# Optimization experiments

Hardware: AMD Instinct MI355X
Metric: run time of the kernel (lower is better)

## Reference

```python
import jax, jax.numpy as jnp
import numpy as np

B, S, D = 4, 4096, 768

def setup_inputs() -> dict:
    key = jax.random.key(0)
    kx, kq, kk, kv = jax.random.split(key, 4)
    x = jax.random.normal(kx, (B, S, D), dtype=jnp.float32)
    Wq = jax.random.normal(kq, (D, D), dtype=jnp.float32) * (D ** -0.5)
    Wk = jax.random.normal(kk, (D, D), dtype=jnp.float32) * (D ** -0.5)
    Wv = jax.random.normal(kv, (D, D), dtype=jnp.float32) * (D ** -0.5)
    return {"x": x, "Wq": Wq, "Wk": Wk, "Wv": Wv}

def reference(x, Wq, Wk, Wv):
    # q,k,v: [B,S,D]  (Linear with no bias)
    q = x @ Wq
    k = x @ Wk
    v = x @ Wv
    # full N x N causal score matrix, as in the original module
    scores = jnp.einsum('bqd,bkd->bqk', q, k)  # [B,S,S]
    seq = scores.shape[1]
    causal_mask = jnp.triu(jnp.ones((seq, seq), dtype=bool), k=1)  # True above diagonal
    scores = jnp.where(causal_mask[None, :, :], -jnp.inf, scores)
    scale = jnp.asarray(k.shape[-1], scores.dtype) ** 0.5
    weights = jax.nn.softmax(scores / scale, axis=-1)  # [B,S,S]
    # dropout p=0.0 -> identity (deterministic reference)
    context = jnp.einsum('bqk,bkd->bqd', weights, v)  # [B,S,D]
    return context
```

## Files before the change

kernel.cpp:

```cpp
#include <hip/hip_runtime.h>
#include <hip/hip_bf16.h>

typedef __attribute__((ext_vector_type(8))) _Float16 half8_t;
typedef __attribute__((ext_vector_type(4))) _Float16 half4_t;
typedef __attribute__((ext_vector_type(4))) float float4_t;

#define D_DIM 768
#define S_DIM 4096
#define B_DIM 4
#define M_DIM (B_DIM * S_DIM)
#define SD ((size_t)S_DIM * D_DIM)

#define GLOAD_LDS16(g, s)                                      \
  __builtin_amdgcn_global_load_lds(                            \
      (const __attribute__((address_space(1))) void*)(g),      \
      (__attribute__((address_space(3))) void*)(s), 16, 0, 0)

__device__ __forceinline__ float4_t mfma16(half8_t a, half8_t b, float4_t c) {
  return __builtin_amdgcn_mfma_f32_16x16x32_f16(a, b, c, 0, 0, 0);
}

__global__ __launch_bounds__(256) void cvt_x_kernel(const float* __restrict__ in,
                                                    _Float16* __restrict__ out, int n) {
  int i = (blockIdx.x * 256 + threadIdx.x) * 4;
  if (i < n) {
    float4 v = *(const float4*)(in + i);
    half4_t o;
    o.x = (_Float16)v.x; o.y = (_Float16)v.y; o.z = (_Float16)v.z; o.w = (_Float16)v.w;
    *(half4_t*)(out + i) = o;
  }
}

__global__ __launch_bounds__(256) void transpose_w_kernel(const float* __restrict__ W0,
                                                          const float* __restrict__ W1,
                                                          const float* __restrict__ W2,
                                                          _Float16* __restrict__ WT) {
  const float* W = (blockIdx.z == 0) ? W0 : (blockIdx.z == 1) ? W1 : W2;
  _Float16* o = WT + (size_t)blockIdx.z * D_DIM * D_DIM;
  __shared__ _Float16 tile[64][68];
  int k0 = blockIdx.x * 64, n0 = blockIdx.y * 64;
#pragma unroll
  for (int i = 0; i < 16; ++i) {
    int idx = threadIdx.x + i * 256;
    int r = idx >> 6, c = idx & 63;
    tile[r][c] = (_Float16)W[(size_t)(k0 + r) * D_DIM + n0 + c];
  }
  __syncthreads();
#pragma unroll
  for (int i = 0; i < 16; ++i) {
    int idx = threadIdx.x + i * 256;
    int r = idx >> 6, c = idx & 63;
    o[(size_t)(n0 + r) * D_DIM + k0 + c] = tile[c][r];
  }
}

template <bool SWAP>
__device__ __forceinline__ void core256p(const _Float16* __restrict__ Ag,
                                         const _Float16* __restrict__ Bg,
                                         int lda, int ldb, int nt,
                                         char* lds, float4_t (&acc)[8][4]) {
  const int tid = threadIdx.x;
  const int w = tid >> 6, l = tid & 63;
  const int wm = w >> 2, wn = w & 3;
  const int l15 = l & 15, l4 = l >> 4;

  int sRow[2], sU[2], sDst[2];
#pragma unroll
  for (int i = 0; i < 2; ++i) {
    int L = i * 512 + tid;
    int row = L >> 3, u = L & 7;
    sRow[i] = row;
    sU[i] = (u ^ (row & 7)) * 8;
    sDst[i] = (i * 512 + (tid & ~63)) * 16;
  }

  const int a7 = l15 & 7;
  const int kt0 = ((0 * 4 + l4) ^ a7) * 16;
  const int kt1 = ((1 * 4 + l4) ^ a7) * 16;
  const int aBase = (wm * 128 + l15) * 128;
  const int bBase = 32768 + (wn * 64 + l15) * 128;

#define STGP(t)                                                                 \
  do {                                                                          \
    char* base = lds + ((t) & 1) * 65536;                                       \
    const _Float16* As = Ag + (size_t)(t) * 64;                                 \
    const _Float16* Bs = Bg + (size_t)(t) * 64;                                 \
    _Pragma("unroll") for (int i = 0; i < 2; ++i)                               \
        GLOAD_LDS16(As + (size_t)sRow[i] * lda + sU[i], base + sDst[i]);        \
    _Pragma("unroll") for (int i = 0; i < 2; ++i)                               \
        GLOAD_LDS16(As + (size_t)(sRow[i] + 128) * lda + sU[i],                 \
                    base + 16384 + sDst[i]);                                    \
    _Pragma("unroll") for (int i = 0; i < 2; ++i)                               \
        GLOAD_LDS16(Bs + (size_t)sRow[i] * ldb + sU[i], base + 32768 + sDst[i]);\
    _Pragma("unroll") for (int i = 0; i < 2; ++i)                               \
        GLOAD_LDS16(Bs + (size_t)(sRow[i] + 128) * ldb + sU[i],                 \
                    base + 49152 + sDst[i]);                                    \
  } while (0)

  STGP(0);

#pragma unroll 1
  for (int t = 0; t < nt; ++t) {
    asm volatile("s_waitcnt vmcnt(0)" ::: "memory");
    __builtin_amdgcn_s_barrier();
    __builtin_amdgcn_sched_barrier(0);
    if (t + 1 < nt) STGP(t + 1);
    __builtin_amdgcn_sched_barrier(0);

    const char* Lb = lds + (t & 1) * 65536;
    const char* pA0 = Lb + aBase + kt0;
    const char* pA1 = Lb + aBase + kt1;
    const char* pB0 = Lb + bBase + kt0;
    const char* pB1 = Lb + bBase + kt1;

    half8_t bf[4][2];
#pragma unroll
    for (int ni = 0; ni < 4; ++ni) {
      bf[ni][0] = *(const half8_t*)(pB0 + ni * 2048);
      bf[ni][1] = *(const half8_t*)(pB1 + ni * 2048);
    }

#pragma unroll
    for (int q = 0; q < 4; ++q) {
      if (q) {
        __builtin_amdgcn_s_barrier();
        __builtin_amdgcn_sched_barrier(0);
      }
      half8_t af[2][2];
#pragma unroll
      for (int di = 0; di < 2; ++di) {
        af[di][0] = *(const half8_t*)(pA0 + (q * 2 + di) * 2048);
        af[di][1] = *(const half8_t*)(pA1 + (q * 2 + di) * 2048);
      }
      __builtin_amdgcn_s_setprio(1);
#pragma unroll
      for (int di = 0; di < 2; ++di)
#pragma unroll
        for (int ni = 0; ni < 4; ++ni)
#pragma unroll
          for (int ks = 0; ks < 2; ++ks) {
            if (SWAP)
              acc[q * 2 + di][ni] = mfma16(bf[ni][ks], af[di][ks], acc[q * 2 + di][ni]);
            else
              acc[q * 2 + di][ni] = mfma16(af[di][ks], bf[ni][ks], acc[q * 2 + di][ni]);
          }
      __builtin_amdgcn_s_setprio(0);
    }
    __builtin_amdgcn_s_barrier();
  }
#undef STGP
}

template <bool SWAP>
__device__ __forceinline__ void core128(const _Float16* __restrict__ Ag,
                                        const _Float16* __restrict__ Bg,
                                        int lda, int ldb, int nt,
                                        char* lds, float4_t (&acc)[4][4]) {
  const int tid = threadIdx.x;
  const int w = tid >> 6, l = tid & 63;
  const int wr = w >> 1, wc = w & 1;
  const int l15 = l & 15, l4 = l >> 4;

  int sA[4], sB[4], sDst[4];
#pragma unroll
  for (int i = 0; i < 4; ++i) {
    int L = i * 256 + tid;
    int row = L >> 3, u = L & 7;
    int usw = u ^ (row & 7);
    sA[i] = row * lda + usw * 8;
    sB[i] = row * ldb + usw * 8;
    sDst[i] = (i * 256 + (tid & ~63)) * 16;
  }

  int aOff[2][4], bOff[2][4];
#pragma unroll
  for (int ks = 0; ks < 2; ++ks) {
#pragma unroll
    for (int i = 0; i < 4; ++i) {
      int ar = wr * 64 + i * 16 + l15;
      aOff[ks][i] = ar * 128 + (((ks * 4 + l4) ^ (ar & 7)) * 16);
      int br = wc * 64 + i * 16 + l15;
      bOff[ks][i] = 16384 + br * 128 + (((ks * 4 + l4) ^ (br & 7)) * 16);
    }
  }

#pragma unroll 1
  for (int kt = 0; kt < nt; ++kt) {
#pragma unroll
    for (int i = 0; i < 4; ++i)
      GLOAD_LDS16(Ag + (size_t)kt * 64 + sA[i], lds + sDst[i]);
#pragma unroll
    for (int i = 0; i < 4; ++i)
      GLOAD_LDS16(Bg + (size_t)kt * 64 + sB[i], lds + 16384 + sDst[i]);
    __syncthreads();
#pragma unroll
    for (int ks = 0; ks < 2; ++ks) {
      half8_t af[4], bf[4];
#pragma unroll
      for (int ni = 0; ni < 4; ++ni) bf[ni] = *(const half8_t*)(lds + bOff[ks][ni]);
#pragma unroll
      for (int mi = 0; mi < 4; ++mi) af[mi] = *(const half8_t*)(lds + aOff[ks][mi]);
      __builtin_amdgcn_s_setprio(1);
#pragma unroll
      for (int mi = 0; mi < 4; ++mi)
#pragma unroll
        for (int ni = 0; ni < 4; ++ni) {
          if (SWAP)
            acc[mi][ni] = mfma16(bf[ni], af[mi], acc[mi][ni]);
          else
            acc[mi][ni] = mfma16(af[mi], bf[ni], acc[mi][ni]);
        }
      __builtin_amdgcn_s_setprio(0);
    }
    __syncthreads();
  }
}

__global__ __launch_bounds__(512) void proj8_kernel(const _Float16* __restrict__ xh,
                                                    const _Float16* __restrict__ WT,
                                                    _Float16* __restrict__ qkv,
                                                    _Float16* __restrict__ vt) {
  __shared__ __align__(16) char lds[131072];
  const int bid = blockIdx.x;
  const int wid = (bid & 7) * 72 + (bid >> 3);
  const int rg2 = wid / 18;
  const int rem = wid % 18;
  const int z = rem / 6;
  const int cb = (rem % 6) >> 1;
  const int rbg = rg2 * 2 + (rem & 1);

  const _Float16* Ag = xh + (size_t)rbg * 256 * D_DIM;
  const _Float16* Bg = WT + (size_t)z * D_DIM * D_DIM + (size_t)cb * 256 * D_DIM;
  float4_t acc[8][4];
#pragma unroll
  for (int a = 0; a < 8; ++a)
#pragma unroll
    for (int b = 0; b < 4; ++b) acc[a][b] = (float4_t){0.f, 0.f, 0.f, 0.f};

  const int tid = threadIdx.x;
  const int w = tid >> 6, l = tid & 63;
  const int wr = w >> 2, wc = w & 3;
  const int l15 = l & 15, l4 = l >> 4;

  if (z < 2) {
    core256p<false>(Ag, Bg, D_DIM, D_DIM, 12, lds, acc);
    _Float16* C = qkv + (size_t)z * M_DIM * D_DIM;
#pragma unroll
    for (int mi = 0; mi < 8; ++mi)
#pragma unroll
      for (int ni = 0; ni < 4; ++ni) {
        int col = cb * 256 + wc * 64 + ni * 16 + l15;
#pragma unroll
        for (int j = 0; j < 4; ++j) {
          int row = rbg * 256 + wr * 128 + mi * 16 + l4 * 4 + j;
          C[(size_t)row * D_DIM + col] = (_Float16)acc[mi][ni][j];
        }
      }
  } else {
    core256p<true>(Ag, Bg, D_DIM, D_DIM, 12, lds, acc);
#pragma unroll
    for (int mi = 0; mi < 8; ++mi) {
      int scol = rbg * 256 + wr * 128 + mi * 16 + l15;
      int bb = scol >> 12;
      int sl = scol & 4095;
      _Float16* vtb = vt + (size_t)bb * SD;
#pragma unroll
      for (int ni = 0; ni < 4; ++ni) {
#pragma unroll
        for (int j = 0; j < 4; ++j) {
          int drow = cb * 256 + wc * 64 + ni * 16 + l4 * 4 + j;
          vtb[(size_t)drow * S_DIM + sl] = (_Float16)acc[mi][ni][j];
        }
      }
    }
  }
}

__global__ __launch_bounds__(512) void gemm1_8_kernel(const _Float16* __restrict__ Q,
                                                      const _Float16* __restrict__ K,
                                                      _Float16* __restrict__ P,
                                                      float* __restrict__ rp) {
  __shared__ __align__(16) char lds[131072];
  const float SCALE = 0.036084391824351615f;
  const int bid = blockIdx.x;
  const int wid = (bid & 7) * 68 + (bid >> 3);
  const int z = wid / 136;
  const int t = wid % 136;
  int g, base;
  if (t < 10) { g = 0; base = 0; }
  else if (t < 36) { g = 1; base = 10; }
  else if (t < 78) { g = 2; base = 36; }
  else { g = 3; base = 78; }
  int r = t - base;
  int rbg, cb;
  if (r < 16 * g) {
    int cbg = r >> 4, wi = r & 15;
    rbg = 4 * g + (wi >> 2);
    cb = 4 * cbg + (wi & 3);
  } else {
    int r2 = r - 16 * g;
    const int ri[10] = {0, 1, 1, 2, 2, 2, 3, 3, 3, 3};
    const int rj[10] = {0, 0, 1, 0, 1, 2, 0, 1, 2, 3};
    rbg = 4 * g + ri[r2];
    cb = 4 * g + rj[r2];
  }

  const _Float16* Ag = Q + (size_t)z * SD + (size_t)rbg * 256 * D_DIM;
  const _Float16* Bg = K + (size_t)z * SD + (size_t)cb * 256 * D_DIM;
  float4_t acc[8][4];
#pragma unroll
  for (int a = 0; a < 8; ++a)
#pragma unroll
    for (int b = 0; b < 4; ++b) acc[a][b] = (float4_t){0.f, 0.f, 0.f, 0.f};
  core256p<false>(Ag, Bg, D_DIM, D_DIM, 12, lds, acc);

  const int tid = threadIdx.x;
  const int w = tid >> 6, l = tid & 63;
  const int wr = w >> 2, wc = w & 3;
  const int l15 = l & 15, l4 = l >> 4;
  _Float16* Pz = P + (size_t)z * S_DIM * S_DIM;
  float* rpz = rp + (size_t)z * S_DIM * 64;
#pragma unroll
  for (int mi = 0; mi < 8; ++mi) {
#pragma unroll
    for (int j = 0; j < 4; ++j) {
      int row = rbg * 256 + wr * 128 + mi * 16 + l4 * 4 + j;
      float rs = 0.f;
#pragma unroll
      for (int ni = 0; ni < 4; ++ni) {
        int col = cb * 256 + wc * 64 + ni * 16 + l15;
        float v = (col <= row) ? __expf(acc[mi][ni][j] * SCALE - 4.0f) : 0.f;
        _Float16 ph = (_Float16)v;
        Pz[(size_t)row * S_DIM + col] = ph;
        rs += (float)ph;
      }
#pragma unroll
      for (int d = 1; d < 16; d <<= 1) rs += __shfl_xor(rs, d);
      if (l15 == 0) rpz[(size_t)row * 64 + cb * 4 + wc] = rs;
    }
  }
}

__global__ __launch_bounds__(256) void rsum_combine_kernel(const float* __restrict__ rp,
                                                           float* __restrict__ rsum) {
  int idx = blockIdx.x * 256 + threadIdx.x;
  int row = idx & 4095;
  int np = ((row >> 8) + 1) * 4;
  const float* p = rp + (size_t)idx * 64;
  float s = 0.f;
  for (int i = 0; i < np; ++i) s += p[i];
  rsum[idx] = s;
}

__global__ __launch_bounds__(256) void gemm2_8_kernel(const _Float16* __restrict__ P,
                                                      const _Float16* __restrict__ VT,
                                                      float* __restrict__ outp,
                                                      const float* __restrict__ rsum) {
  __shared__ __align__(16) char lds[32768];
  const int bid = blockIdx.x;
  const int g = bid / 24;
  const int q = bid % 24;
  const int rbg = 31 - g;
  const int xcd = q & 7;
  const int slot = q >> 3;
  const int z = xcd >> 1;
  const int by = (xcd & 1) * 3 + slot;
  const int nt = 2 * (rbg + 1);

  const _Float16* Ag = P + (size_t)z * S_DIM * S_DIM + (size_t)rbg * 128 * S_DIM;
  const _Float16* Bg = VT + (size_t)z * SD + (size_t)by * 128 * S_DIM;
  float4_t acc[4][4];
#pragma unroll
  for (int a = 0; a < 4; ++a)
#pragma unroll
    for (int b = 0; b < 4; ++b) acc[a][b] = (float4_t){0.f, 0.f, 0.f, 0.f};
  core128<false>(Ag, Bg, S_DIM, S_DIM, nt, lds, acc);

  const int tid = threadIdx.x;
  const int w = tid >> 6, l = tid & 63;
  const int wr = w >> 1, wc = w & 1;
  const int l15 = l & 15, l4 = l >> 4;
#pragma unroll
  for (int mi = 0; mi < 4; ++mi) {
#pragma unroll
    for (int j = 0; j < 4; ++j) {
      int row = rbg * 128 + wr * 64 + mi * 16 + l4 * 4 + j;
      float rinv = 1.0f / rsum[(size_t)z * S_DIM + row];
#pragma unroll
      for (int ni = 0; ni < 4; ++ni) {
        int col = by * 128 + wc * 64 + ni * 16 + l15;
        outp[(size_t)z * SD + (size_t)row * D_DIM + col] = acc[mi][ni][j] * rinv;
      }
    }
  }
}

extern "C" void kernel_launch(void* const* d_in, const int* in_sizes, int n_in,
                              void* d_out, int out_size, void* d_ws, size_t ws_size,
                              hipStream_t stream) {
  const float* x = (const float*)d_in[0];
  const float* Wq = (const float*)d_in[1];
  const float* Wk = (const float*)d_in[2];
  const float* Wv = (const float*)d_in[3];
  float* out = (float*)d_out;
  char* ws = (char*)d_ws;

  const size_t XH_B = (size_t)M_DIM * D_DIM * 2;
  const size_t QKV_B = 3 * XH_B;
  const size_t VT_B = XH_B;
  const size_t WT_B = (size_t)3 * D_DIM * D_DIM * 2;
  const size_t BASE_END = XH_B + QKV_B + VT_B + WT_B;

  _Float16* xh = (_Float16*)ws;
  _Float16* qkv = (_Float16*)(ws + XH_B);
  _Float16* Q = qkv;
  _Float16* K = qkv + (size_t)M_DIM * D_DIM;
  _Float16* vt = (_Float16*)(ws + XH_B + QKV_B);
  _Float16* wt = (_Float16*)(ws + XH_B + QKV_B + VT_B);

  float* rp = (float*)(ws + BASE_END);
  float* rsum = (float*)(ws + BASE_END + (size_t)4194304);
  _Float16* P = (_Float16*)(ws + BASE_END + (size_t)4259840);

  cvt_x_kernel<<<dim3(12288), dim3(256), 0, stream>>>(x, xh, M_DIM * D_DIM);
  transpose_w_kernel<<<dim3(12, 12, 3), dim3(256), 0, stream>>>(Wq, Wk, Wv, wt);
  proj8_kernel<<<dim3(576), dim3(512), 0, stream>>>(xh, wt, qkv, vt);
  gemm1_8_kernel<<<dim3(544), dim3(512), 0, stream>>>(Q, K, P, rp);
  rsum_combine_kernel<<<dim3(64), dim3(256), 0, stream>>>(rp, rsum);
  gemm2_8_kernel<<<dim3(768), dim3(256), 0, stream>>>(P, vt, out, rsum);
}
```

Before: 275.9 us.

## Deepen GEMM load pipeline with split-stage prefetch and fuse small prep/rsum kernels

Rewrites the 256-tile GEMM core so global-to-LDS loads for the next tiles are split into four quarter-stages interleaved with the MFMA phases, using partial vmcnt waits instead of a full drain each iteration. It also merges the x conversion and weight transpose into one prep launch, and folds the row-sum combine into the gemm2 epilogue through shared memory, removing two launches. Launch bounds now request 2 waves per SIMD on the big kernels. The finer schedule relies on exact vmcnt counts and adds barriers, and the fused rsum adds serial loads to the gemm2 epilogue.

New measurement: 278.7 us. Within noise of the previous version (+1.0%).

```diff
diff --git a/kernel.cpp b/kernel.cpp
--- a/kernel.cpp
+++ b/kernel.cpp
@@ -20,42 +20,46 @@
   return __builtin_amdgcn_mfma_f32_16x16x32_f16(a, b, c, 0, 0, 0);
 }
 
-__global__ __launch_bounds__(256) void cvt_x_kernel(const float* __restrict__ in,
-                                                    _Float16* __restrict__ out, int n) {
-  int i = (blockIdx.x * 256 + threadIdx.x) * 4;
-  if (i < n) {
-    float4 v = *(const float4*)(in + i);
+__global__ __launch_bounds__(256) void prep_kernel(const float* __restrict__ x,
+                                                   const float* __restrict__ W0,
+                                                   const float* __restrict__ W1,
+                                                   const float* __restrict__ W2,
+                                                   _Float16* __restrict__ xh,
+                                                   _Float16* __restrict__ WT) {
+  __shared__ _Float16 tile[64][68];
+  const int bid = blockIdx.x;
+  if (bid < 12288) {
+    int i = (bid * 256 + threadIdx.x) * 4;
+    float4 v = *(const float4*)(x + i);
     half4_t o;
     o.x = (_Float16)v.x; o.y = (_Float16)v.y; o.z = (_Float16)v.z; o.w = (_Float16)v.w;
-    *(half4_t*)(out + i) = o;
-  }
-}
-
-__global__ __launch_bounds__(256) void transpose_w_kernel(const float* __restrict__ W0,
-                                                          const float* __restrict__ W1,
-                                                          const float* __restrict__ W2,
-                                                          _Float16* __restrict__ WT) {
-  const float* W = (blockIdx.z == 0) ? W0 : (blockIdx.z == 1) ? W1 : W2;
-  _Float16* o = WT + (size_t)blockIdx.z * D_DIM * D_DIM;
-  __shared__ _Float16 tile[64][68];
-  int k0 = blockIdx.x * 64, n0 = blockIdx.y * 64;
-#pragma unroll
-  for (int i = 0; i < 16; ++i) {
-    int idx = threadIdx.x + i * 256;
-    int r = idx >> 6, c = idx & 63;
-    tile[r][c] = (_Float16)W[(size_t)(k0 + r) * D_DIM + n0 + c];
-  }
-  __syncthreads();
-#pragma unroll
-  for (int i = 0; i < 16; ++i) {
-    int idx = threadIdx.x + i * 256;
-    int r = idx >> 6, c = idx & 63;
-    o[(size_t)(n0 + r) * D_DIM + k0 + c] = tile[c][r];
+    *(half4_t*)(xh + i) = o;
+  } else {
+    int t = bid - 12288;
+    int z = t / 144;
+    int r = t % 144;
+    int kx = r / 12, ny = r % 12;
+    const float* W = (z == 0) ? W0 : (z == 1) ? W1 : W2;
+    _Float16* o = WT + (size_t)z * D_DIM * D_DIM;
+    int k0 = kx * 64, n0 = ny * 64;
+#pragma unroll
+    for (int i = 0; i < 16; ++i) {
+      int idx = threadIdx.x + i * 256;
+      int rr = idx >> 6, cc = idx & 63;
+      tile[rr][cc] = (_Float16)W[(size_t)(k0 + rr) * D_DIM + n0 + cc];
+    }
+    __syncthreads();
+#pragma unroll
+    for (int i = 0; i < 16; ++i) {
+      int idx = threadIdx.x + i * 256;
+      int rr = idx >> 6, cc = idx & 63;
+      o[(size_t)(n0 + rr) * D_DIM + k0 + cc] = tile[cc][rr];
+    }
   }
 }
 
 template <bool SWAP>
-__device__ __forceinline__ void core256p(const _Float16* __restrict__ Ag,
+__device__ __forceinline__ void core256f(const _Float16* __restrict__ Ag,
                                          const _Float16* __restrict__ Bg,
                                          int lda, int ldb, int nt,
                                          char* lds, float4_t (&acc)[8][4]) {
@@ -64,91 +68,152 @@
   const int wm = w >> 2, wn = w & 3;
   const int l15 = l & 15, l4 = l >> 4;
 
-  int sRow[2], sU[2], sDst[2];
+  int srcB0[2], srcB1[2], srcAX[2], srcAY[2], dstLin[2];
 #pragma unroll
   for (int i = 0; i < 2; ++i) {
-    int L = i * 512 + tid;
-    int row = L >> 3, u = L & 7;
-    sRow[i] = row;
-    sU[i] = (u ^ (row & 7)) * 8;
-    sDst[i] = (i * 512 + (tid & ~63)) * 16;
-  }
+    int g = i * 512 + tid;
+    int r = g >> 3, u = g & 7;
+    int usw = (u ^ (r & 7)) * 8;
+    srcB0[i] = r * ldb + usw;
+    srcB1[i] = (r + 128) * ldb + usw;
+    srcAX[i] = (r + (i ? 64 : 0)) * lda + usw;
+    srcAY[i] = (r + 64 + (i ? 64 : 0)) * lda + usw;
+    dstLin[i] = (i * 512 + (tid & ~63)) * 16;
+  }
+
+#define STG_B0(t)                                                       \
+  do {                                                                  \
+    char* bb = lds + ((t) & 1) * 65536 + 32768;                         \
+    const _Float16* s = Bg + (size_t)(t) * 64;                          \
+    GLOAD_LDS16(s + srcB0[0], bb + dstLin[0]);                          \
+    GLOAD_LDS16(s + srcB0[1], bb + dstLin[1]);                          \
+  } while (0)
+#define STG_B1(t)                                                       \
+  do {                                                                  \
+    char* bb = lds + ((t) & 1) * 65536 + 49152;                         \
+    const _Float16* s = Bg + (size_t)(t) * 64;                          \
+    GLOAD_LDS16(s + srcB1[0], bb + dstLin[0]);                          \
+    GLOAD_LDS16(s + srcB1[1], bb + dstLin[1]);                          \
+  } while (0)
+#define STG_AX(t)                                                       \
+  do {                                                                  \
+    char* bb = lds + ((t) & 1) * 65536;                                 \
+    const _Float16* s = Ag + (size_t)(t) * 64;                          \
+    GLOAD_LDS16(s + srcAX[0], bb + dstLin[0]);                          \
+    GLOAD_LDS16(s + srcAX[1], bb + dstLin[1] + 8192);                   \
+  } while (0)
+#define STG_AY(t)                                                       \
+  do {                                                                  \
+    char* bb = lds + ((t) & 1) * 65536;                                 \
+    const _Float16* s = Ag + (size_t)(t) * 64;                          \
+    GLOAD_LDS16(s + srcAY[0], bb + dstLin[0] + 8192);                   \
+    GLOAD_LDS16(s + srcAY[1], bb + dstLin[1] + 16384);                  \
+  } while (0)
 
   const int a7 = l15 & 7;
-  const int kt0 = ((0 * 4 + l4) ^ a7) * 16;
-  const int kt1 = ((1 * 4 + l4) ^ a7) * 16;
-  const int aBase = (wm * 128 + l15) * 128;
-  const int bBase = 32768 + (wn * 64 + l15) * 128;
-
-#define STGP(t)                                                                 \
-  do {                                                                          \
-    char* base = lds + ((t) & 1) * 65536;                                       \
-    const _Float16* As = Ag + (size_t)(t) * 64;                                 \
-    const _Float16* Bs = Bg + (size_t)(t) * 64;                                 \
-    _Pragma("unroll") for (int i = 0; i < 2; ++i)                               \
-        GLOAD_LDS16(As + (size_t)sRow[i] * lda + sU[i], base + sDst[i]);        \
-    _Pragma("unroll") for (int i = 0; i < 2; ++i)                               \
-        GLOAD_LDS16(As + (size_t)(sRow[i] + 128) * lda + sU[i],                 \
-                    base + 16384 + sDst[i]);                                    \
-    _Pragma("unroll") for (int i = 0; i < 2; ++i)                               \
-        GLOAD_LDS16(Bs + (size_t)sRow[i] * ldb + sU[i], base + 32768 + sDst[i]);\
-    _Pragma("unroll") for (int i = 0; i < 2; ++i)                               \
-        GLOAD_LDS16(Bs + (size_t)(sRow[i] + 128) * ldb + sU[i],                 \
-                    base + 49152 + sDst[i]);                                    \
-  } while (0)
-
-  STGP(0);
+  int aBase[2], bBase[2];
+#pragma unroll
+  for (int ks = 0; ks < 2; ++ks) {
+    int kk = ((ks * 4 + l4) ^ a7) * 16;
+    aBase[ks] = wm * 16384 + l15 * 128 + kk;
+    bBase[ks] = 32768 + wn * 8192 + l15 * 128 + kk;
+  }
+
+  STG_B0(0); STG_B1(0); STG_AX(0); STG_AY(0);
+  if (nt > 1) {
+    STG_B0(1); STG_B1(1); STG_AX(1);
+    asm volatile("s_waitcnt vmcnt(6)" ::: "memory");
+  } else {
+    asm volatile("s_waitcnt vmcnt(0)" ::: "memory");
+  }
+  __builtin_amdgcn_s_barrier();
+
+  half8_t bf[2][4];
+
+  auto do_mfma = [&](int mh, int ks, half8_t (&af)[4]) {
+    __builtin_amdgcn_s_setprio(1);
+#pragma unroll
+    for (int i = 0; i < 4; ++i)
+#pragma unroll
+      for (int n = 0; n < 4; ++n) {
+        if (SWAP)
+          acc[mh * 4 + i][n] = mfma16(bf[ks][n], af[i], acc[mh * 4 + i][n]);
+        else
+          acc[mh * 4 + i][n] = mfma16(af[i], bf[ks][n], acc[mh * 4 + i][n]);
+      }
+    __builtin_amdgcn_s_setprio(0);
+  };
 
 #pragma unroll 1
   for (int t = 0; t < nt; ++t) {
-    asm volatile("s_waitcnt vmcnt(0)" ::: "memory");
-    __builtin_amdgcn_s_barrier();
-    __builtin_amdgcn_sched_barrier(0);
-    if (t + 1 < nt) STGP(t + 1);
-    __builtin_amdgcn_sched_barrier(0);
-
     const char* Lb = lds + (t & 1) * 65536;
-    const char* pA0 = Lb + aBase + kt0;
-    const char* pA1 = Lb + aBase + kt1;
-    const char* pB0 = Lb + bBase + kt0;
-    const char* pB1 = Lb + bBase + kt1;
-
-    half8_t bf[4][2];
-#pragma unroll
-    for (int ni = 0; ni < 4; ++ni) {
-      bf[ni][0] = *(const half8_t*)(pB0 + ni * 2048);
-      bf[ni][1] = *(const half8_t*)(pB1 + ni * 2048);
-    }
-
-#pragma unroll
-    for (int q = 0; q < 4; ++q) {
-      if (q) {
-        __builtin_amdgcn_s_barrier();
-        __builtin_amdgcn_sched_barrier(0);
-      }
-      half8_t af[2][2];
-#pragma unroll
-      for (int di = 0; di < 2; ++di) {
-        af[di][0] = *(const half8_t*)(pA0 + (q * 2 + di) * 2048);
-        af[di][1] = *(const half8_t*)(pA1 + (q * 2 + di) * 2048);
-      }
-      __builtin_amdgcn_s_setprio(1);
-#pragma unroll
-      for (int di = 0; di < 2; ++di)
-#pragma unroll
-        for (int ni = 0; ni < 4; ++ni)
-#pragma unroll
-          for (int ks = 0; ks < 2; ++ks) {
-            if (SWAP)
-              acc[q * 2 + di][ni] = mfma16(bf[ni][ks], af[di][ks], acc[q * 2 + di][ni]);
-            else
-              acc[q * 2 + di][ni] = mfma16(af[di][ks], bf[ni][ks], acc[q * 2 + di][ni]);
-          }
-      __builtin_amdgcn_s_setprio(0);
-    }
-    __builtin_amdgcn_s_barrier();
-  }
-#undef STGP
+    {
+      half8_t af[4];
+#pragma unroll
+      for (int ks = 0; ks < 2; ++ks)
+#pragma unroll
+        for (int n = 0; n < 4; ++n)
+          bf[ks][n] = *(const half8_t*)(Lb + bBase[ks] + n * 2048);
+#pragma unroll
+      for (int i = 0; i < 4; ++i)
+        af[i] = *(const half8_t*)(Lb + aBase[0] + i * 2048);
+      if (t + 1 < nt) STG_AY(t + 1);
+      __builtin_amdgcn_sched_barrier(0);
+      __builtin_amdgcn_s_barrier();
+      __builtin_amdgcn_sched_barrier(0);
+      do_mfma(0, 0, af);
+      __builtin_amdgcn_sched_barrier(0);
+      __builtin_amdgcn_s_barrier();
+    }
+    {
+      half8_t af[4];
+#pragma unroll
+      for (int i = 0; i < 4; ++i)
+        af[i] = *(const half8_t*)(Lb + aBase[0] + (4 + i) * 2048);
+      if (t + 2 < nt) STG_B0(t + 2);
+      __builtin_amdgcn_sched_barrier(0);
+      __builtin_amdgcn_s_barrier();
+      __builtin_amdgcn_sched_barrier(0);
+      do_mfma(1, 0, af);
+      __builtin_amdgcn_sched_barrier(0);
+      __builtin_amdgcn_s_barrier();
+    }
+    {
+      half8_t af[4];
+#pragma unroll
+      for (int i = 0; i < 4; ++i)
+        af[i] = *(const half8_t*)(Lb + aBase[1] + i * 2048);
+      if (t + 2 < nt) STG_B1(t + 2);
+      __builtin_amdgcn_sched_barrier(0);
+      __builtin_amdgcn_s_barrier();
+      __builtin_amdgcn_sched_barrier(0);
+      do_mfma(0, 1, af);
+      __builtin_amdgcn_sched_barrier(0);
+      __builtin_amdgcn_s_barrier();
+    }
+    {
+      half8_t af[4];
+#pragma unroll
+      for (int i = 0; i < 4; ++i)
+        af[i] = *(const half8_t*)(Lb + aBase[1] + (4 + i) * 2048);
+      if (t + 2 < nt) STG_AX(t + 2);
+      __builtin_amdgcn_sched_barrier(0);
+      __builtin_amdgcn_s_barrier();
+      __builtin_amdgcn_sched_barrier(0);
+      do_mfma(1, 1, af);
+      __builtin_amdgcn_sched_barrier(0);
+      if (t + 2 < nt)
+        asm volatile("s_waitcnt vmcnt(6)" ::: "memory");
+      else if (t + 1 < nt)
+        asm volatile("s_waitcnt vmcnt(0)" ::: "memory");
+      __builtin_amdgcn_sched_barrier(0);
+      __builtin_amdgcn_s_barrier();
+    }
+  }
+#undef STG_B0
+#undef STG_B1
+#undef STG_AX
+#undef STG_AY
 }
 
 template <bool SWAP>
@@ -216,10 +281,10 @@
   }
 }
 
-__global__ __launch_bounds__(512) void proj8_kernel(const _Float16* __restrict__ xh,
-                                                    const _Float16* __restrict__ WT,
-                                                    _Float16* __restrict__ qkv,
-                                                    _Float16* __restrict__ vt) {
+__global__ __launch_bounds__(512, 2) void proj8_kernel(const _Float16* __restrict__ xh,
+                                                       const _Float16* __restrict__ WT,
+                                                       _Float16* __restrict__ qkv,
+                                                       _Float16* __restrict__ vt) {
   __shared__ __align__(16) char lds[131072];
   const int bid = blockIdx.x;
   const int wid = (bid & 7) * 72 + (bid >> 3);
@@ -243,7 +308,7 @@
   const int l15 = l & 15, l4 = l >> 4;
 
   if (z < 2) {
-    core256p<false>(Ag, Bg, D_DIM, D_DIM, 12, lds, acc);
+    core256f<false>(Ag, Bg, D_DIM, D_DIM, 12, lds, acc);
     _Float16* C = qkv + (size_t)z * M_DIM * D_DIM;
 #pragma unroll
     for (int mi = 0; mi < 8; ++mi)
@@ -257,7 +322,7 @@
         }
       }
   } else {
-    core256p<true>(Ag, Bg, D_DIM, D_DIM, 12, lds, acc);
+    core256f<true>(Ag, Bg, D_DIM, D_DIM, 12, lds, acc);
 #pragma unroll
     for (int mi = 0; mi < 8; ++mi) {
       int scol = rbg * 256 + wr * 128 + mi * 16 + l15;
@@ -276,10 +341,10 @@
   }
 }
 
-__global__ __launch_bounds__(512) void gemm1_8_kernel(const _Float16* __restrict__ Q,
-                                                      const _Float16* __restrict__ K,
-                                                      _Float16* __restrict__ P,
-                                                      float* __restrict__ rp) {
+__global__ __launch_bounds__(512, 2) void gemm1_8_kernel(const _Float16* __restrict__ Q,
+                                                         const _Float16* __restrict__ K,
+                                                         _Float16* __restrict__ P,
+                                                         float* __restrict__ rp) {
   __shared__ __align__(16) char lds[131072];
   const float SCALE = 0.036084391824351615f;
   const int bid = blockIdx.x;
@@ -312,7 +377,7 @@
   for (int a = 0; a < 8; ++a)
 #pragma unroll
     for (int b = 0; b < 4; ++b) acc[a][b] = (float4_t){0.f, 0.f, 0.f, 0.f};
-  core256p<false>(Ag, Bg, D_DIM, D_DIM, 12, lds, acc);
+  core256f<false>(Ag, Bg, D_DIM, D_DIM, 12, lds, acc);
 
   const int tid = threadIdx.x;
   const int w = tid >> 6, l = tid & 63;
@@ -341,22 +406,12 @@
   }
 }
 
-__global__ __launch_bounds__(256) void rsum_combine_kernel(const float* __restrict__ rp,
-                                                           float* __restrict__ rsum) {
-  int idx = blockIdx.x * 256 + threadIdx.x;
-  int row = idx & 4095;
-  int np = ((row >> 8) + 1) * 4;
-  const float* p = rp + (size_t)idx * 64;
-  float s = 0.f;
-  for (int i = 0; i < np; ++i) s += p[i];
-  rsum[idx] = s;
-}
-
 __global__ __launch_bounds__(256) void gemm2_8_kernel(const _Float16* __restrict__ P,
                                                       const _Float16* __restrict__ VT,
                                                       float* __restrict__ outp,
-                                                      const float* __restrict__ rsum) {
+                                                      const float* __restrict__ rp) {
   __shared__ __align__(16) char lds[32768];
+  __shared__ float rsm[128];
   const int bid = blockIdx.x;
   const int g = bid / 24;
   const int q = bid % 24;
@@ -377,6 +432,14 @@
   core128<false>(Ag, Bg, S_DIM, S_DIM, nt, lds, acc);
 
   const int tid = threadIdx.x;
+  if (tid < 128) {
+    const float* p = rp + ((size_t)z * S_DIM + (size_t)rbg * 128 + tid) * 64;
+    float s = 0.f;
+    for (int i = 0; i < nt; ++i) s += p[i];
+    rsm[tid] = 1.0f / s;
+  }
+  __syncthreads();
+
   const int w = tid >> 6, l = tid & 63;
   const int wr = w >> 1, wc = w & 1;
   const int l15 = l & 15, l4 = l >> 4;
@@ -384,8 +447,9 @@
   for (int mi = 0; mi < 4; ++mi) {
 #pragma unroll
     for (int j = 0; j < 4; ++j) {
-      int row = rbg * 128 + wr * 64 + mi * 16 + l4 * 4 + j;
-      float rinv = 1.0f / rsum[(size_t)z * S_DIM + row];
+      int lrow = wr * 64 + mi * 16 + l4 * 4 + j;
+      int row = rbg * 128 + lrow;
+      float rinv = rsm[lrow];
 #pragma unroll
       for (int ni = 0; ni < 4; ++ni) {
         int col = by * 128 + wc * 64 + ni * 16 + l15;
@@ -419,13 +483,10 @@
   _Float16* wt = (_Float16*)(ws + XH_B + QKV_B + VT_B);
 
   float* rp = (float*)(ws + BASE_END);
-  float* rsum = (float*)(ws + BASE_END + (size_t)4194304);
   _Float16* P = (_Float16*)(ws + BASE_END + (size_t)4259840);
 
-  cvt_x_kernel<<<dim3(12288), dim3(256), 0, stream>>>(x, xh, M_DIM * D_DIM);
-  transpose_w_kernel<<<dim3(12, 12, 3), dim3(256), 0, stream>>>(Wq, Wk, Wv, wt);
+  prep_kernel<<<dim3(12720), dim3(256), 0, stream>>>(x, Wq, Wk, Wv, xh, wt);
   proj8_kernel<<<dim3(576), dim3(512), 0, stream>>>(xh, wt, qkv, vt);
   gemm1_8_kernel<<<dim3(544), dim3(512), 0, stream>>>(Q, K, P, rp);
-  rsum_combine_kernel<<<dim3(64), dim3(256), 0, stream>>>(rp, rsum);
-  gemm2_8_kernel<<<dim3(768), dim3(256), 0, stream>>>(P, vt, out, rsum);
-}
+  gemm2_8_kernel<<<dim3(768), dim3(256), 0, stream>>>(P, vt, out, rp);
+}
```
